# Kernel optimization log

Hardware: AMD Instinct MI355X
Metric: run time of the kernel (lower is better)

## Reference

```python
import jax, jax.numpy as jnp
import numpy as np

EMBED_DIM = 1024
NUM_HEADS = 16
HEAD_DIM = EMBED_DIM // NUM_HEADS
SPARSITY_LAMBDA = 0.01
B, S = 2, 2048


def setup_inputs() -> dict:
    key = jax.random.key(0)
    ks = jax.random.split(key, 10)
    scale = 0.02
    inp = {
        "x": jax.random.normal(ks[0], (B, S, EMBED_DIM), dtype=jnp.float32),
        "Wq": jax.random.normal(ks[1], (EMBED_DIM, EMBED_DIM), dtype=jnp.float32) * scale,
        "bq": jnp.zeros((EMBED_DIM,), dtype=jnp.float32),
        "Wk": jax.random.normal(ks[2], (EMBED_DIM, EMBED_DIM), dtype=jnp.float32) * scale,
        "bk": jnp.zeros((EMBED_DIM,), dtype=jnp.float32),
        "Wv": jax.random.normal(ks[3], (EMBED_DIM, EMBED_DIM), dtype=jnp.float32) * scale,
        "bv": jnp.zeros((EMBED_DIM,), dtype=jnp.float32),
        "Wo": jax.random.normal(ks[4], (EMBED_DIM, EMBED_DIM), dtype=jnp.float32) * scale,
        "bo": jnp.zeros((EMBED_DIM,), dtype=jnp.float32),
        "z": jax.random.normal(ks[5], (NUM_HEADS,), dtype=jnp.float32),
    }
    return inp


def reference(x, Wq, bq, Wk, bk, Wv, bv, Wo, bo, z):
    # Linear layers (torch Linear: y = x @ W.T + b); W here stored as [out, in]
    def split_heads(t):  # [B,S,E] -> [B,H,S,D]
        return t.reshape(B, S, NUM_HEADS, HEAD_DIM).transpose(0, 2, 1, 3)

    q = split_heads(x @ Wq.T + bq)
    k = split_heads(x @ Wk.T + bk)
    v = split_heads(x @ Wv.T + bv)

    scores = jnp.einsum("bhsd,bhtd->bhst", q, k) / jnp.sqrt(jnp.float32(HEAD_DIM))
    gate = jax.nn.sigmoid(z)  # [H], per-head scalar gate on raw scores
    scores = scores * gate[None, :, None, None]
    probs = jax.nn.softmax(scores, axis=-1)
    ctx = jnp.einsum("bhst,bhtd->bhsd", probs, v)  # [B,H,S,D]
    ctx = ctx.transpose(0, 2, 1, 3).reshape(B, S, EMBED_DIM)
    out = ctx @ Wo.T + bo
    penalty = jnp.sum(jax.nn.sigmoid(z)) * SPARSITY_LAMBDA
    return out, penalty
```

## Files before the change

### kernel.cpp

```cpp
#include <hip/hip_runtime.h>

typedef unsigned short ushort_t;
typedef __bf16 bf16x8 __attribute__((ext_vector_type(8)));
typedef ushort_t u16x8 __attribute__((ext_vector_type(8)));
typedef float f32x4 __attribute__((ext_vector_type(4)));

#define DEVI __device__ __forceinline__

constexpr int Ed = 1024;
constexpr int Hh = 16;
constexpr int Dd = 64;
constexpr int Ss = 2048;
constexpr int Mm = 4096;

constexpr int NX4 = Mm * Ed / 4;
constexpr int NW4 = Ed * Ed / 4;

DEVI ushort_t f2bf(float f) {
    union { float f; unsigned int i; } v; v.f = f;
    unsigned int r = v.i + 0x7fffu + ((v.i >> 16) & 1u);
    return (ushort_t)(r >> 16);
}

__global__ __launch_bounds__(256) void cvt_all(
    const float* __restrict__ x,  const float* __restrict__ Wq,
    const float* __restrict__ Wk, const float* __restrict__ Wv,
    const float* __restrict__ Wo,
    ushort_t* __restrict__ xb,  ushort_t* __restrict__ Wqb,
    ushort_t* __restrict__ Wkb, ushort_t* __restrict__ Wvb,
    ushort_t* __restrict__ Wob)
{
    int i = blockIdx.x * 256 + threadIdx.x;
    const float* s; ushort_t* d; int off;
    if (i < NX4)                { s = x;  d = xb;  off = i; }
    else if (i < NX4 + NW4)     { s = Wq; d = Wqb; off = i - NX4; }
    else if (i < NX4 + 2 * NW4) { s = Wk; d = Wkb; off = i - NX4 - NW4; }
    else if (i < NX4 + 3 * NW4) { s = Wv; d = Wvb; off = i - NX4 - 2 * NW4; }
    else                        { s = Wo; d = Wob; off = i - NX4 - 3 * NW4; }
    float4 v = ((const float4*)s)[off];
    ushort4 o; o.x = f2bf(v.x); o.y = f2bf(v.y); o.z = f2bf(v.z); o.w = f2bf(v.w);
    ((ushort4*)d)[off] = o;
}

DEVI void gld16(const void* g, void* l) {
    __builtin_amdgcn_global_load_lds(
        (__attribute__((address_space(1))) void*)(g),
        (__attribute__((address_space(3))) void*)(l), 16, 0, 0);
}

DEVI void gemm_core(const ushort_t* __restrict__ A, const ushort_t* __restrict__ W,
                    ushort_t* As, ushort_t* Bs, int tm, int tn, int K,
                    f32x4 acc[4][4])
{
    const int tid  = threadIdx.x;
    const int w    = tid >> 6;
    const int lane = tid & 63;
    const int quad = lane >> 4;
    const int l15  = lane & 15;
    const int wy   = w >> 1, wx = w & 1;
    const int rowc = lane >> 3;
    const int col8 = (lane & 7) * 8;

    for (int k0 = 0; k0 < K; k0 += 64) {
        __syncthreads();
#pragma unroll
        for (int i = 0; i < 4; ++i) {
            int chunk = w * 4 + i;
            int row = chunk * 8 + rowc;
            gld16(A + (size_t)(tm + row) * K + k0 + col8, (char*)As + chunk * 1024);
            gld16(W + (size_t)(tn + row) * K + k0 + col8, (char*)Bs + chunk * 1024);
        }
        __syncthreads();
#pragma unroll
        for (int ks = 0; ks < 64; ks += 32) {
            bf16x8 a[4], b[4];
#pragma unroll
            for (int mi = 0; mi < 4; ++mi)
                a[mi] = *(const bf16x8*)&As[(wy * 64 + mi * 16 + l15) * 64 + ks + quad * 8];
#pragma unroll
            for (int ni = 0; ni < 4; ++ni)
                b[ni] = *(const bf16x8*)&Bs[(wx * 64 + ni * 16 + l15) * 64 + ks + quad * 8];
#pragma unroll
            for (int mi = 0; mi < 4; ++mi)
#pragma unroll
                for (int ni = 0; ni < 4; ++ni)
                    acc[mi][ni] = __builtin_amdgcn_mfma_f32_16x16x32_bf16(
                        a[mi], b[ni], acc[mi][ni], 0, 0, 0);
        }
    }
}

__global__ __launch_bounds__(256, 2) void qkv_gemm(
    const ushort_t* __restrict__ x,
    const ushort_t* __restrict__ Wq, const float* __restrict__ bq,
    const ushort_t* __restrict__ Wk, const float* __restrict__ bk,
    const ushort_t* __restrict__ Wv, const float* __restrict__ bv,
    ushort_t* __restrict__ qo, ushort_t* __restrict__ ko, ushort_t* __restrict__ vto)
{
    __shared__ __align__(16) ushort_t As[128 * 64];
    __shared__ __align__(16) ushort_t Bs[128 * 64];
    const ushort_t* W; const float* bias; ushort_t* outp; int vmode;
    if (blockIdx.z == 0)      { W = Wq; bias = bq; outp = qo;  vmode = 0; }
    else if (blockIdx.z == 1) { W = Wk; bias = bk; outp = ko;  vmode = 0; }
    else                      { W = Wv; bias = bv; outp = vto; vmode = 1; }

    const int tm = blockIdx.x * 128, tn = blockIdx.y * 128;
    f32x4 acc[4][4] = {};
    gemm_core(x, W, As, Bs, tm, tn, Ed, acc);

    const int tid = threadIdx.x, w = tid >> 6, lane = tid & 63;
    const int quad = lane >> 4, l15 = lane & 15;
    const int wy = w >> 1, wx = w & 1;
#pragma unroll
    for (int ni = 0; ni < 4; ++ni) {
        int gc = tn + wx * 64 + ni * 16 + l15;
        float bb = bias[gc];
        int h = gc >> 6, d = gc & 63;
#pragma unroll
        for (int mi = 0; mi < 4; ++mi) {
#pragma unroll
            for (int r = 0; r < 4; ++r) {
                int gr = tm + wy * 64 + mi * 16 + quad * 4 + r;
                int b_ = gr >> 11, s_ = gr & 2047;
                float v = acc[mi][ni][r] + bb;
                size_t addr;
                if (vmode == 0) addr = ((size_t)(b_ * Hh + h) * Ss + s_) * Dd + d;
                else            addr = ((size_t)(b_ * Hh + h) * Dd + d) * Ss + s_;
                outp[addr] = f2bf(v);
            }
        }
    }
}

__global__ __launch_bounds__(256, 2) void out_gemm(
    const ushort_t* __restrict__ ctx, const ushort_t* __restrict__ Wo,
    const float* __restrict__ bo, float* __restrict__ out)
{
    __shared__ __align__(16) ushort_t As[128 * 64];
    __shared__ __align__(16) ushort_t Bs[128 * 64];
    const int tm = blockIdx.x * 128, tn = blockIdx.y * 128;
    f32x4 acc[4][4] = {};
    gemm_core(ctx, Wo, As, Bs, tm, tn, Ed, acc);

    const int tid = threadIdx.x, w = tid >> 6, lane = tid & 63;
    const int quad = lane >> 4, l15 = lane & 15;
    const int wy = w >> 1, wx = w & 1;
#pragma unroll
    for (int ni = 0; ni < 4; ++ni) {
        int gc = tn + wx * 64 + ni * 16 + l15;
        float bb = bo[gc];
#pragma unroll
        for (int mi = 0; mi < 4; ++mi)
#pragma unroll
            for (int r = 0; r < 4; ++r) {
                int gr = tm + wy * 64 + mi * 16 + quad * 4 + r;
                out[(size_t)gr * Ed + gc] = acc[mi][ni][r] + bb;
            }
    }
}

__global__ __launch_bounds__(256, 4) void attn(
    const ushort_t* __restrict__ Q, const ushort_t* __restrict__ Kk,
    const ushort_t* __restrict__ Vt, const float* __restrict__ z,
    ushort_t* __restrict__ ctx)
{
    __shared__ __align__(16) ushort_t Ks[64 * 64];
    __shared__ __align__(16) ushort_t Vs[64 * 64];
    __shared__ __align__(16) ushort_t Ps[4][16 * 68];

    const int tid = threadIdx.x, w = tid >> 6, lane = tid & 63;
    const int quad = lane >> 4, l15 = lane & 15;
    const int qt = blockIdx.x;
    const int bh = blockIdx.y;
    const int h = bh & (Hh - 1), b_ = bh >> 4;
    const size_t base = (size_t)bh * Ss * Dd;

    const float gate = 1.f / (1.f + __expf(-z[h]));
    const float scl2 = gate * 0.125f * 1.44269504f;

    bf16x8 aQ[2];
#pragma unroll
    for (int c = 0; c < 2; ++c)
        aQ[c] = *(const bf16x8*)&Q[base + (size_t)(qt * 64 + w * 16 + l15) * Dd
                                   + c * 32 + quad * 8];

    const int rowA = w * 16 + (lane >> 3);
    const int rowB = rowA + 8;
    const int gsA  = (lane & 7) ^ (rowA & 7);
    const int gsB  = (lane & 7) ^ (rowB & 7);
    const ushort_t* kSrcA = Kk + base + (size_t)rowA * Dd + gsA * 8;
    const ushort_t* kSrcB = Kk + base + (size_t)rowB * Dd + gsB * 8;
    const ushort_t* vSrcA = Vt + base + (size_t)rowA * Ss + gsA * 8;
    const ushort_t* vSrcB = Vt + base + (size_t)rowB * Ss + gsB * 8;
    ushort_t* kDstA = Ks + (w * 2) * 512;
    ushort_t* kDstB = Ks + (w * 2 + 1) * 512;
    ushort_t* vDstA = Vs + (w * 2) * 512;
    ushort_t* vDstB = Vs + (w * 2 + 1) * 512;

    f32x4 accO[4] = {};
    float lsum[4] = {0.f, 0.f, 0.f, 0.f};

    const int swq = (l15 & 7) * 8;

    for (int kt = 0; kt < Ss / 64; ++kt) {
        __syncthreads();
        gld16(kSrcA + (size_t)kt * 64 * Dd, kDstA);
        gld16(kSrcB + (size_t)kt * 64 * Dd, kDstB);
        gld16(vSrcA + kt * 64, vDstA);
        gld16(vSrcB + kt * 64, vDstB);
        __syncthreads();

        f32x4 sAcc[4] = {};
#pragma unroll
        for (int ni = 0; ni < 4; ++ni) {
            bf16x8 b0 = *(const bf16x8*)&Ks[(ni * 16 + l15) * 64 + ((quad ^ 0) * 8 ^ swq)];
            bf16x8 b1 = *(const bf16x8*)&Ks[(ni * 16 + l15) * 64 + ((quad + 4) * 8 ^ swq)];
            sAcc[ni] = __builtin_amdgcn_mfma_f32_16x16x32_bf16(aQ[0], b0, sAcc[ni], 0, 0, 0);
            sAcc[ni] = __builtin_amdgcn_mfma_f32_16x16x32_bf16(aQ[1], b1, sAcc[ni], 0, 0, 0);
        }

#pragma unroll
        for (int ni = 0; ni < 4; ++ni)
#pragma unroll
            for (int r = 0; r < 4; ++r) {
                float p = exp2f(sAcc[ni][r] * scl2);
                lsum[r] += p;
                Ps[w][(quad * 4 + r) * 68 + ni * 16 + l15] = f2bf(p);
            }

#pragma unroll
        for (int c = 0; c < 2; ++c) {
            bf16x8 aP = *(const bf16x8*)&Ps[w][l15 * 68 + c * 32 + quad * 8];
#pragma unroll
            for (int ni = 0; ni < 4; ++ni) {
                bf16x8 bV = *(const bf16x8*)&Vs[(ni * 16 + l15) * 64 + (((quad + 4 * c) * 8) ^ swq)];
                accO[ni] = __builtin_amdgcn_mfma_f32_16x16x32_bf16(aP, bV, accO[ni], 0, 0, 0);
            }
        }
    }

#pragma unroll
    for (int r = 0; r < 4; ++r) {
        lsum[r] += __shfl_xor(lsum[r], 1);
        lsum[r] += __shfl_xor(lsum[r], 2);
        lsum[r] += __shfl_xor(lsum[r], 4);
        lsum[r] += __shfl_xor(lsum[r], 8);
    }

#pragma unroll
    for (int r = 0; r < 4; ++r) {
        int srow = qt * 64 + w * 16 + quad * 4 + r;
        float inv = 1.f / lsum[r];
#pragma unroll
        for (int ni = 0; ni < 4; ++ni) {
            int d = ni * 16 + l15;
            ctx[((size_t)(b_ * Ss + srow)) * Ed + h * Dd + d] = f2bf(accO[ni][r] * inv);
        }
    }
}

__global__ void penalty_k(const float* __restrict__ z, float* __restrict__ out) {
    if (threadIdx.x == 0) {
        float s = 0.f;
        for (int h = 0; h < Hh; ++h) s += 1.f / (1.f + __expf(-z[h]));
        out[(size_t)Mm * Ed] = s * 0.01f;
    }
}

extern "C" void kernel_launch(void* const* d_in, const int* in_sizes, int n_in,
                              void* d_out, int out_size, void* d_ws, size_t ws_size,
                              hipStream_t stream) {
    const float* x  = (const float*)d_in[0];
    const float* Wq = (const float*)d_in[1];
    const float* bq = (const float*)d_in[2];
    const float* Wk = (const float*)d_in[3];
    const float* bk = (const float*)d_in[4];
    const float* Wv = (const float*)d_in[5];
    const float* bv = (const float*)d_in[6];
    const float* Wo = (const float*)d_in[7];
    const float* bo = (const float*)d_in[8];
    const float* z  = (const float*)d_in[9];
    float* out = (float*)d_out;

    ushort_t* xb  = (ushort_t*)d_ws;
    ushort_t* Wqb = xb  + (size_t)Mm * Ed;
    ushort_t* Wkb = Wqb + (size_t)Ed * Ed;
    ushort_t* Wvb = Wkb + (size_t)Ed * Ed;
    ushort_t* Wob = Wvb + (size_t)Ed * Ed;
    ushort_t* qw  = Wob + (size_t)Ed * Ed;
    ushort_t* kw  = qw + (size_t)Mm * Ed;
    ushort_t* vT  = kw + (size_t)Mm * Ed;
    ushort_t* cx  = vT + (size_t)Mm * Ed;

    dim3 blk(256);
    cvt_all<<<dim3((NX4 + 4 * NW4) / 256), blk, 0, stream>>>(
        x, Wq, Wk, Wv, Wo, xb, Wqb, Wkb, Wvb, Wob);
    qkv_gemm<<<dim3(Mm / 128, Ed / 128, 3), blk, 0, stream>>>(
        xb, Wqb, bq, Wkb, bk, Wvb, bv, qw, kw, vT);
    attn<<<dim3(Ss / 64, 2 * Hh), blk, 0, stream>>>(qw, kw, vT, z, cx);
    out_gemm<<<dim3(Mm / 128, Ed / 128), blk, 0, stream>>>(cx, Wob, bo, out);
    penalty_k<<<1, 64, 0, stream>>>(z, out);
}
```

Measured before the change: 230.9 us.

## Double attention query tile per block and load V fragments directly from global

The attention kernel now processes 128 query rows per block (32 per wave), so each K tile staged in shared memory is reused across twice as many queries and the grid halves. V is no longer staged in shared memory; each lane loads its V^T fragments straight from global into registers every key tile. This raises register pressure (launch bounds lowered to 2 blocks/SM) and makes V reads uncoalesced-ish per-lane global loads, possibly redundant across waves, trading LDS traffic for global/L2 traffic and lower occupancy.

```diff
diff --git a/kernel.cpp b/kernel.cpp
--- a/kernel.cpp
+++ b/kernel.cpp
@@ -159,14 +159,13 @@
     }
 }
 
-__global__ __launch_bounds__(256, 4) void attn(
+__global__ __launch_bounds__(256, 2) void attn(
     const ushort_t* __restrict__ Q, const ushort_t* __restrict__ Kk,
     const ushort_t* __restrict__ Vt, const float* __restrict__ z,
     ushort_t* __restrict__ ctx)
 {
     __shared__ __align__(16) ushort_t Ks[64 * 64];
-    __shared__ __align__(16) ushort_t Vs[64 * 64];
-    __shared__ __align__(16) ushort_t Ps[4][16 * 68];
+    __shared__ __align__(16) ushort_t Ps[4][32 * 68];
 
     const int tid = threadIdx.x, w = tid >> 6, lane = tid & 63;
     const int quad = lane >> 4, l15 = lane & 15;
@@ -178,11 +177,13 @@
     const float gate = 1.f / (1.f + __expf(-z[h]));
     const float scl2 = gate * 0.125f * 1.44269504f;
 
-    bf16x8 aQ[2];
-#pragma unroll
-    for (int c = 0; c < 2; ++c)
-        aQ[c] = *(const bf16x8*)&Q[base + (size_t)(qt * 64 + w * 16 + l15) * Dd
-                                   + c * 32 + quad * 8];
+    bf16x8 aQ[2][2];
+#pragma unroll
+    for (int mi = 0; mi < 2; ++mi)
+#pragma unroll
+        for (int c = 0; c < 2; ++c)
+            aQ[mi][c] = *(const bf16x8*)&Q[base
+                + (size_t)(qt * 128 + w * 32 + mi * 16 + l15) * Dd + c * 32 + quad * 8];
 
     const int rowA = w * 16 + (lane >> 3);
     const int rowB = rowA + 8;
@@ -190,15 +191,11 @@
     const int gsB  = (lane & 7) ^ (rowB & 7);
     const ushort_t* kSrcA = Kk + base + (size_t)rowA * Dd + gsA * 8;
     const ushort_t* kSrcB = Kk + base + (size_t)rowB * Dd + gsB * 8;
-    const ushort_t* vSrcA = Vt + base + (size_t)rowA * Ss + gsA * 8;
-    const ushort_t* vSrcB = Vt + base + (size_t)rowB * Ss + gsB * 8;
     ushort_t* kDstA = Ks + (w * 2) * 512;
     ushort_t* kDstB = Ks + (w * 2 + 1) * 512;
-    ushort_t* vDstA = Vs + (w * 2) * 512;
-    ushort_t* vDstB = Vs + (w * 2 + 1) * 512;
-
-    f32x4 accO[4] = {};
-    float lsum[4] = {0.f, 0.f, 0.f, 0.f};
+
+    f32x4 accO[2][4] = {};
+    float lsum[2][4] = {};
 
     const int swq = (l15 & 7) * 8;
 
@@ -206,57 +203,72 @@
         __syncthreads();
         gld16(kSrcA + (size_t)kt * 64 * Dd, kDstA);
         gld16(kSrcB + (size_t)kt * 64 * Dd, kDstB);
-        gld16(vSrcA + kt * 64, vDstA);
-        gld16(vSrcB + kt * 64, vDstB);
+        bf16x8 bV[4][2];
+#pragma unroll
+        for (int ni = 0; ni < 4; ++ni)
+#pragma unroll
+            for (int c = 0; c < 2; ++c)
+                bV[ni][c] = *(const bf16x8*)&Vt[base
+                    + (size_t)(ni * 16 + l15) * Ss + kt * 64 + c * 32 + quad * 8];
         __syncthreads();
 
-        f32x4 sAcc[4] = {};
+        f32x4 sAcc[2][4] = {};
 #pragma unroll
         for (int ni = 0; ni < 4; ++ni) {
-            bf16x8 b0 = *(const bf16x8*)&Ks[(ni * 16 + l15) * 64 + ((quad ^ 0) * 8 ^ swq)];
-            bf16x8 b1 = *(const bf16x8*)&Ks[(ni * 16 + l15) * 64 + ((quad + 4) * 8 ^ swq)];
-            sAcc[ni] = __builtin_amdgcn_mfma_f32_16x16x32_bf16(aQ[0], b0, sAcc[ni], 0, 0, 0);
-            sAcc[ni] = __builtin_amdgcn_mfma_f32_16x16x32_bf16(aQ[1], b1, sAcc[ni], 0, 0, 0);
-        }
-
-#pragma unroll
-        for (int ni = 0; ni < 4; ++ni)
-#pragma unroll
-            for (int r = 0; r < 4; ++r) {
-                float p = exp2f(sAcc[ni][r] * scl2);
-                lsum[r] += p;
-                Ps[w][(quad * 4 + r) * 68 + ni * 16 + l15] = f2bf(p);
-            }
-
-#pragma unroll
-        for (int c = 0; c < 2; ++c) {
-            bf16x8 aP = *(const bf16x8*)&Ps[w][l15 * 68 + c * 32 + quad * 8];
+            bf16x8 b0 = *(const bf16x8*)&Ks[(ni * 16 + l15) * 64 + ((quad * 8) ^ swq)];
+            bf16x8 b1 = *(const bf16x8*)&Ks[(ni * 16 + l15) * 64 + (((quad + 4) * 8) ^ swq)];
+#pragma unroll
+            for (int mi = 0; mi < 2; ++mi) {
+                sAcc[mi][ni] = __builtin_amdgcn_mfma_f32_16x16x32_bf16(aQ[mi][0], b0, sAcc[mi][ni], 0, 0, 0);
+                sAcc[mi][ni] = __builtin_amdgcn_mfma_f32_16x16x32_bf16(aQ[mi][1], b1, sAcc[mi][ni], 0, 0, 0);
+            }
+        }
+
+#pragma unroll
+        for (int mi = 0; mi < 2; ++mi)
+#pragma unroll
+            for (int ni = 0; ni < 4; ++ni)
+#pragma unroll
+                for (int r = 0; r < 4; ++r) {
+                    float p = exp2f(sAcc[mi][ni][r] * scl2);
+                    lsum[mi][r] += p;
+                    Ps[w][(mi * 16 + quad * 4 + r) * 68 + ni * 16 + l15] = f2bf(p);
+                }
+
+#pragma unroll
+        for (int c = 0; c < 2; ++c)
+#pragma unroll
+            for (int mi = 0; mi < 2; ++mi) {
+                bf16x8 aP = *(const bf16x8*)&Ps[w][(mi * 16 + l15) * 68 + c * 32 + quad * 8];
+#pragma unroll
+                for (int ni = 0; ni < 4; ++ni)
+                    accO[mi][ni] = __builtin_amdgcn_mfma_f32_16x16x32_bf16(
+                        aP, bV[ni][c], accO[mi][ni], 0, 0, 0);
+            }
+    }
+
+#pragma unroll
+    for (int mi = 0; mi < 2; ++mi)
+#pragma unroll
+        for (int r = 0; r < 4; ++r) {
+            lsum[mi][r] += __shfl_xor(lsum[mi][r], 1);
+            lsum[mi][r] += __shfl_xor(lsum[mi][r], 2);
+            lsum[mi][r] += __shfl_xor(lsum[mi][r], 4);
+            lsum[mi][r] += __shfl_xor(lsum[mi][r], 8);
+        }
+
+#pragma unroll
+    for (int mi = 0; mi < 2; ++mi)
+#pragma unroll
+        for (int r = 0; r < 4; ++r) {
+            int srow = qt * 128 + w * 32 + mi * 16 + quad * 4 + r;
+            float inv = 1.f / lsum[mi][r];
 #pragma unroll
             for (int ni = 0; ni < 4; ++ni) {
-                bf16x8 bV = *(const bf16x8*)&Vs[(ni * 16 + l15) * 64 + (((quad + 4 * c) * 8) ^ swq)];
-                accO[ni] = __builtin_amdgcn_mfma_f32_16x16x32_bf16(aP, bV, accO[ni], 0, 0, 0);
-            }
-        }
-    }
-
-#pragma unroll
-    for (int r = 0; r < 4; ++r) {
-        lsum[r] += __shfl_xor(lsum[r], 1);
-        lsum[r] += __shfl_xor(lsum[r], 2);
-        lsum[r] += __shfl_xor(lsum[r], 4);
-        lsum[r] += __shfl_xor(lsum[r], 8);
-    }
-
-#pragma unroll
-    for (int r = 0; r < 4; ++r) {
-        int srow = qt * 64 + w * 16 + quad * 4 + r;
-        float inv = 1.f / lsum[r];
-#pragma unroll
-        for (int ni = 0; ni < 4; ++ni) {
-            int d = ni * 16 + l15;
-            ctx[((size_t)(b_ * Ss + srow)) * Ed + h * Dd + d] = f2bf(accO[ni][r] * inv);
-        }
-    }
+                int d = ni * 16 + l15;
+                ctx[((size_t)(b_ * Ss + srow)) * Ed + h * Dd + d] = f2bf(accO[mi][ni][r] * inv);
+            }
+        }
 }
 
 __global__ void penalty_k(const float* __restrict__ z, float* __restrict__ out) {
@@ -297,7 +309,7 @@
         x, Wq, Wk, Wv, Wo, xb, Wqb, Wkb, Wvb, Wob);
     qkv_gemm<<<dim3(Mm / 128, Ed / 128, 3), blk, 0, stream>>>(
         xb, Wqb, bq, Wkb, bk, Wvb, bv, qw, kw, vT);
-    attn<<<dim3(Ss / 64, 2 * Hh), blk, 0, stream>>>(qw, kw, vT, z, cx);
+    attn<<<dim3(Ss / 128, 2 * Hh), blk, 0, stream>>>(qw, kw, vT, z, cx);
     out_gemm<<<dim3(Mm / 128, Ed / 128), blk, 0, stream>>>(cx, Wob, bo, out);
     penalty_k<<<1, 64, 0, stream>>>(z, out);
 }
```

Result: slower. 247.3 us (+7.1%).
